# Kernel optimization log

Measured on AMD Instinct MI355X. Metric: run time of the kernel, lower is better.

The kernel has to match this reference:

```python
import jax, jax.numpy as jnp
import numpy as np

B, S, D, H = 2, 2048, 768, 12
DK = D // H


def setup_inputs() -> dict:
    key = jax.random.key(0)
    ks = jax.random.split(key, 10)
    sc = 0.02
    return {
        "k": jax.random.normal(ks[0], (B, S, D), jnp.float32),
        "q": jax.random.normal(ks[1], (B, S, D), jnp.float32),
        "v": jax.random.normal(ks[2], (B, S, D), jnp.float32),
        "mask": jnp.ones((B, 1, S, S), jnp.int32),
        "wq": jax.random.normal(ks[3], (D, D), jnp.float32) * sc,
        "bq": jnp.zeros((D,), jnp.float32),
        "wk": jax.random.normal(ks[4], (D, D), jnp.float32) * sc,
        "bk": jnp.zeros((D,), jnp.float32),
        "wv": jax.random.normal(ks[5], (D, D), jnp.float32) * sc,
        "bv": jnp.zeros((D,), jnp.float32),
        "wo": jax.random.normal(ks[6], (D, D), jnp.float32) * sc,
        "bo": jnp.zeros((D,), jnp.float32),
    }


def reference(k, q, v, mask, wq, bq, wk, bk, wv, bv, wo, bo):
    # Linear projections (torch Linear: x @ W^T + b)
    query = q @ wq.T + bq
    key_ = k @ wk.T + bk
    value = v @ wv.T + bv
    # [B,S,D] -> [B,H,S,DK]
    def split_heads(x):
        return x.reshape(B, S, H, DK).transpose(0, 2, 1, 3)
    Q, K, V = split_heads(query), split_heads(key_), split_heads(value)
    # NOTE: original masked_fill result is discarded -> mask is a no-op.
    scores = jnp.einsum("bhqd,bhkd->bhqk", Q, K) / jnp.sqrt(jnp.float32(DK))
    attn = jax.nn.softmax(scores, axis=-1)  # dropout p=0.0 -> identity
    out = jnp.einsum("bhqk,bhkd->bhqd", attn, V)
    out = out.transpose(0, 2, 1, 3).reshape(B, S, D)
    return out @ wo.T + bo
```

## Files before the change

kernel.cpp:

```cpp
#include <hip/hip_runtime.h>
#include <hip/hip_bf16.h>

#define B_  2
#define S_  2048
#define D_  768
#define H_  12
#define DK_ 64
#define NX_ (B_*S_*D_)
#define NW_ (D_*D_)
#define CSC 0.18033688011112042f

typedef __attribute__((ext_vector_type(8))) short  bf16x8;
typedef __attribute__((ext_vector_type(4))) float  f32x4;

__device__ __forceinline__ unsigned short f2bf(float f) {
    unsigned int u = __float_as_uint(f);
    u += 0x7fffu + ((u >> 16) & 1u);
    return (unsigned short)(u >> 16);
}

__device__ __forceinline__ unsigned cvtpk(float a, float b) {
    unsigned r;
    asm("v_cvt_pk_bf16_f32 %0, %1, %2" : "=v"(r) : "v"(a), "v"(b));
    return r;
}

__device__ __forceinline__ void async_cp16(const unsigned short* g,
                                           const unsigned short* lds_uniform_base) {
    __builtin_amdgcn_global_load_lds(
        (const __attribute__((address_space(1))) unsigned int*)(uintptr_t)g,
        (__attribute__((address_space(3))) unsigned int*)(unsigned int)(uintptr_t)lds_uniform_base,
        16, 0, 0);
}

struct CvtArgs { const float* s[7]; };

__global__ __launch_bounds__(256) void cvt_all(CvtArgs a,
                                               unsigned short* __restrict__ Xsw,
                                               unsigned short* __restrict__ Wsw) {
    const int bx = blockIdx.x;
    int y, inner;
    if (bx < 2304) { y = bx / 768;             inner = bx % 768; }
    else           { y = 3 + (bx - 2304) / 144; inner = (bx - 2304) % 144; }
    const int idx = inner * 256 + threadIdx.x;
    const int n  = idx / 48;
    const int g2 = idx % 48;
    const float* src = a.s[y] + (long)n * D_ + g2 * 16;
    const float zs = (y == 3) ? CSC : 1.0f;
    unsigned short o[16];
#pragma unroll
    for (int i = 0; i < 4; i++) {
        const float4 f = *(const float4*)(src + i * 4);
        o[i*4+0] = f2bf(f.x*zs); o[i*4+1] = f2bf(f.y*zs);
        o[i*4+2] = f2bf(f.z*zs); o[i*4+3] = f2bf(f.w*zs);
    }
    unsigned short* dst = (y >= 3) ? (Wsw + (long)(y - 3) * NW_ + (long)n * D_)
                                   : (Xsw + (long)y * NX_ + (long)n * D_);
    const int key = n & 7;
#pragma unroll
    for (int h = 0; h < 2; h++) {
        const int g8 = g2 * 2 + h;
        const int kdst = (g8 >> 3) * 64 + (((g8 & 7) ^ key) * 8);
        *(uint4*)(dst + kdst) = *(const uint4*)&o[h * 8];
    }
}

struct QkvArgs { const float* bias[3]; unsigned short* out[3]; };

__global__ __launch_bounds__(256, 3) void gemm_qkv(QkvArgs args,
                                                   const unsigned short* __restrict__ Xsw,
                                                   const unsigned short* __restrict__ Wsw) {
    __shared__ __align__(16) unsigned short smem[17408];
    unsigned short* As = smem;
    unsigned short* Bs = smem + 8192;

    const int t    = threadIdx.x;
    const int wave = t >> 6;
    const int lane = t & 63;
    const int l16  = lane & 15;
    const int quad = lane >> 4;
    const int wm   = wave >> 1, wn = wave & 1;
    const int m0   = blockIdx.x * 128;
    const int zz   = blockIdx.y / 6;
    const int nb   = blockIdx.y % 6;
    const int n0   = nb * 128;

    const unsigned short* Ap = Xsw + (long)zz * NX_;
    const unsigned short* Wp = Wsw + (long)zz * NW_;

    f32x4 acc[4][4];
#pragma unroll
    for (int s = 0; s < 4; s++)
#pragma unroll
        for (int j = 0; j < 4; j++) acc[s][j] = (f32x4){0.f, 0.f, 0.f, 0.f};

    const int lrow = lane >> 3;
    const int lcg  = lane & 7;

    for (int k0 = 0; k0 < D_; k0 += 64) {
        __syncthreads();
#pragma unroll
        for (int i = 0; i < 4; i++) {
            const int chunk = wave * 4 + i;
            async_cp16(Ap + (long)(m0 + chunk * 8 + lrow) * D_ + k0 + lcg * 8,
                       As + chunk * 512);
        }
#pragma unroll
        for (int i = 0; i < 4; i++) {
            const int chunk = wave * 4 + i;
            async_cp16(Wp + (long)(n0 + chunk * 8 + lrow) * D_ + k0 + lcg * 8,
                       Bs + chunk * 512);
        }
        __syncthreads();
#pragma unroll
        for (int ks = 0; ks < 2; ks++) {
            const int cg = ks * 4 + quad;
            bf16x8 af[4], bf[4];
#pragma unroll
            for (int s = 0; s < 4; s++) {
                const int r = wm * 64 + s * 16 + l16;
                af[s] = *(const bf16x8*)&As[r * 64 + ((cg ^ (r & 7)) * 8)];
            }
#pragma unroll
            for (int j = 0; j < 4; j++) {
                const int r = wn * 64 + j * 16 + l16;
                bf[j] = *(const bf16x8*)&Bs[r * 64 + ((cg ^ (r & 7)) * 8)];
            }
#pragma unroll
            for (int s = 0; s < 4; s++)
#pragma unroll
                for (int j = 0; j < 4; j++)
                    acc[s][j] = __builtin_amdgcn_mfma_f32_16x16x32_bf16(af[s], bf[j], acc[s][j], 0, 0, 0);
        }
    }
    __syncthreads();

    const int b     = m0 >> 11;
    const int sbase = m0 & (S_ - 1);
    const float zs  = (zz == 0) ? CSC : 1.0f;
    float bv[4];
#pragma unroll
    for (int j = 0; j < 4; j++) bv[j] = args.bias[zz][n0 + wn * 64 + j * 16 + l16] * zs;

    if (zz < 2) {
        unsigned short* Ls = smem;
#pragma unroll
        for (int s = 0; s < 4; s++)
#pragma unroll
            for (int j = 0; j < 4; j++)
#pragma unroll
                for (int r = 0; r < 4; r++)
                    Ls[(wm * 64 + s * 16 + quad * 4 + r) * 136 + wn * 64 + j * 16 + l16] =
                        f2bf(acc[s][j][r] + bv[j]);
        __syncthreads();
        const int row  = t >> 1;
        const int half = t & 1;
        unsigned short* Op = args.out[zz];
#pragma unroll
        for (int i = 0; i < 8; i++) {
            const int col  = half * 64 + i * 8;
            const int head = nb * 2 + half;
            const uint4 v = *(const uint4*)&Ls[row * 136 + col];
            *(uint4*)(Op + ((long)(b * H_ + head) * S_ + sbase + row) * DK_
                         + ((i ^ (row & 7)) * 8)) = v;
        }
    } else {
        unsigned short* Ls = smem;
#pragma unroll
        for (int s = 0; s < 4; s++)
#pragma unroll
            for (int j = 0; j < 4; j++)
#pragma unroll
                for (int r = 0; r < 4; r++) {
                    const int dk  = j * 16 + l16;
                    const int pos = wm * 64 + (s >> 1) * 32 + quad * 8 + (s & 1) * 4 + r;
                    Ls[wn * 8704 + dk * 136 + pos] = f2bf(acc[s][j][r] + bv[j]);
                }
        __syncthreads();
        const int rowIdx = t >> 1;
        const int hh = rowIdx >> 6, dk = rowIdx & 63;
        const int half = t & 1;
        unsigned short* Op = args.out[2];
#pragma unroll
        for (int i = 0; i < 8; i++) {
            const int col = half * 64 + i * 8;
            const uint4 v = *(const uint4*)&Ls[hh * 8704 + dk * 136 + col];
            const int head = nb * 2 + hh;
            *(uint4*)(Op + ((long)(b * H_ + head) * DK_ + dk) * S_
                         + sbase + half * 64 + ((i ^ (dk & 7)) * 8)) = v;
        }
    }
}

__global__ __launch_bounds__(256, 3) void attn_kernel(
    const unsigned short* __restrict__ Q, const unsigned short* __restrict__ K,
    const unsigned short* __restrict__ Vt, unsigned short* __restrict__ Ao)
{
    const int t    = threadIdx.x;
    const int wave = t >> 6;
    const int lane = t & 63;
    const int l16  = lane & 15;
    const int quad = lane >> 4;
    const int bid  = blockIdx.x;
    const int bh    = bid % 24;
    const int qtile = bid / 24;

    const unsigned short* Qp = Q  + (long)bh * S_ * DK_;
    const unsigned short* Kp = K  + (long)bh * S_ * DK_;
    const unsigned short* Vp = Vt + (long)bh * DK_ * S_;

    __shared__ __align__(16) unsigned short smem[16384];

    const int fkey = l16 & 7;
    const int fo0  = ((quad ^ fkey) * 8);
    const int fo1  = (((4 + quad) ^ fkey) * 8);

    bf16x8 qfrag[2];
    {
        const long qoff = (long)(qtile * 64 + wave * 16 + l16) * DK_;
        qfrag[0] = *(const bf16x8*)(Qp + qoff + fo0);
        qfrag[1] = *(const bf16x8*)(Qp + qoff + fo1);
    }

    const int ci0 = wave * 2;
    const int kd0 = ci0 * 512;
    const unsigned short* gk  = Kp + ci0 * 512 + lane * 8;
    const unsigned short* gv0 = Vp + (long)(ci0 * 8 + (lane >> 3)) * S_ + (lane & 7) * 8;
    const unsigned short* gv1 = gv0 + 8 * S_;

    async_cp16(gk,        smem + kd0);
    async_cp16(gk + 512,  smem + kd0 + 512);
    async_cp16(gv0,       smem + 8192 + kd0);
    async_cp16(gv1,       smem + 8192 + kd0 + 512);
    gk += 4096;  gv0 += 64;  gv1 += 64;

    f32x4 oacc[4];
#pragma unroll
    for (int j = 0; j < 4; j++) oacc[j] = (f32x4){0.f, 0.f, 0.f, 0.f};
    float lsum = 0.f;

    for (int it = 0; it < 32; ++it) {
        const int co = (it & 1) * 4096;
        const int no = 4096 - co;
        __syncthreads();
        const unsigned short* Ks = smem + co;
        const unsigned short* Vs = smem + 8192 + co;

        if (it < 31) {
            async_cp16(gk,        smem + no + kd0);
            async_cp16(gk + 512,  smem + no + kd0 + 512);
            async_cp16(gv0,       smem + 8192 + no + kd0);
            async_cp16(gv1,       smem + 8192 + no + kd0 + 512);
            gk += 4096;  gv0 += 64;  gv1 += 64;
        }

        f32x4 sacc[4];
#pragma unroll
        for (int j = 0; j < 4; j++) sacc[j] = (f32x4){0.f, 0.f, 0.f, 0.f};
#pragma unroll
        for (int ks = 0; ks < 2; ks++) {
            const int fo = ks ? fo1 : fo0;
            const bf16x8 qf = ks ? qfrag[1] : qfrag[0];
#pragma unroll
            for (int j = 0; j < 4; j++) {
                const bf16x8 bf = *(const bf16x8*)&Ks[(j * 16 + l16) * 64 + fo];
                sacc[j] = __builtin_amdgcn_mfma_f32_16x16x32_bf16(bf, qf, sacc[j], 0, 0, 0);
            }
        }

        float p[4][4];
#pragma unroll
        for (int j = 0; j < 4; j++)
#pragma unroll
            for (int r = 0; r < 4; r++)
                p[j][r] = exp2f(sacc[j][r]);
#pragma unroll
        for (int j = 0; j < 4; j++)
            lsum += (p[j][0] + p[j][1]) + (p[j][2] + p[j][3]);
        uint4 pw0, pw1;
        pw0.x = cvtpk(p[0][0], p[0][1]);  pw0.y = cvtpk(p[0][2], p[0][3]);
        pw0.z = cvtpk(p[1][0], p[1][1]);  pw0.w = cvtpk(p[1][2], p[1][3]);
        pw1.x = cvtpk(p[2][0], p[2][1]);  pw1.y = cvtpk(p[2][2], p[2][3]);
        pw1.z = cvtpk(p[3][0], p[3][1]);  pw1.w = cvtpk(p[3][2], p[3][3]);
        const bf16x8 pf0 = *(const bf16x8*)&pw0;
        const bf16x8 pf1 = *(const bf16x8*)&pw1;

#pragma unroll
        for (int ks = 0; ks < 2; ks++) {
            const int fo = ks ? fo1 : fo0;
            const bf16x8 pf = ks ? pf1 : pf0;
#pragma unroll
            for (int j = 0; j < 4; j++) {
                const bf16x8 vf = *(const bf16x8*)&Vs[(j * 16 + l16) * 64 + fo];
                oacc[j] = __builtin_amdgcn_mfma_f32_16x16x32_bf16(pf, vf, oacc[j], 0, 0, 0);
            }
        }
    }

    lsum += __shfl_xor(lsum, 16, 64);
    lsum += __shfl_xor(lsum, 32, 64);
    const float inv = 1.f / lsum;
    float scl[4];
#pragma unroll
    for (int r = 0; r < 4; r++) scl[r] = __shfl(inv, quad * 4 + r, 64);

    __syncthreads();
    unsigned short* Sc = smem;
#pragma unroll
    for (int j = 0; j < 4; j++)
#pragma unroll
        for (int r = 0; r < 4; r++) {
            const int row = wave * 16 + quad * 4 + r;
            const int c   = j * 2 + (l16 >> 3);
            Sc[row * 64 + ((c ^ (row & 7)) * 8) + (l16 & 7)] =
                f2bf(oacc[j][r] * scl[r]);
        }

    const int b = bh / H_, h = bh % H_;
    const int row = t >> 2;
    const int p0  = (t & 3) * 2;
    const int qrow = qtile * 64 + row;
    unsigned short* dst = Ao + (long)(b * S_ + qrow) * D_ + h * DK_;
    *(uint4*)(dst + p0 * 8)       = *(const uint4*)&Sc[row * 64 + p0 * 8];
    *(uint4*)(dst + (p0 + 1) * 8) = *(const uint4*)&Sc[row * 64 + (p0 + 1) * 8];
}

__global__ __launch_bounds__(256, 4) void gemm_out(
    const unsigned short* __restrict__ A, const unsigned short* __restrict__ Wsw,
    const float* __restrict__ bias, float* __restrict__ Out)
{
    __shared__ __align__(16) unsigned short smem[8704];
    unsigned short* As = smem;
    unsigned short* Bs = smem + 4096;

    const int t    = threadIdx.x;
    const int wave = t >> 6;
    const int lane = t & 63;
    const int l16  = lane & 15;
    const int quad = lane >> 4;
    const int wm   = wave >> 1, wn = wave & 1;
    const int m0   = blockIdx.x * 64;
    const int n0   = blockIdx.y * 64;

    f32x4 acc[2][2];
#pragma unroll
    for (int s = 0; s < 2; s++)
#pragma unroll
        for (int j = 0; j < 2; j++) acc[s][j] = (f32x4){0.f, 0.f, 0.f, 0.f};

    const int lrow = lane >> 3;
    const int lcg  = lane & 7;

    for (int k0 = 0; k0 < D_; k0 += 64) {
        __syncthreads();
#pragma unroll
        for (int i = 0; i < 2; i++) {
            const int chunk = wave * 2 + i;
            async_cp16(A + (long)(m0 + chunk * 8 + lrow) * D_ + k0 + lcg * 8,
                       As + chunk * 512);
        }
#pragma unroll
        for (int i = 0; i < 2; i++) {
            const int chunk = wave * 2 + i;
            async_cp16(Wsw + (long)(n0 + chunk * 8 + lrow) * D_ + k0 + lcg * 8,
                       Bs + chunk * 512);
        }
        __syncthreads();
#pragma unroll
        for (int ks = 0; ks < 2; ks++) {
            const int cg = ks * 4 + quad;
            bf16x8 af[2], bf[2];
#pragma unroll
            for (int s = 0; s < 2; s++) {
                const int r = wm * 32 + s * 16 + l16;
                af[s] = *(const bf16x8*)&As[r * 64 + ((cg ^ (r & 7)) * 8)];
            }
#pragma unroll
            for (int j = 0; j < 2; j++) {
                const int r = wn * 32 + j * 16 + l16;
                bf[j] = *(const bf16x8*)&Bs[r * 64 + ((cg ^ (r & 7)) * 8)];
            }
#pragma unroll
            for (int s = 0; s < 2; s++)
#pragma unroll
                for (int j = 0; j < 2; j++)
                    acc[s][j] = __builtin_amdgcn_mfma_f32_16x16x32_bf16(af[s], bf[j], acc[s][j], 0, 0, 0);
        }
    }

    float bv[2];
#pragma unroll
    for (int j = 0; j < 2; j++) bv[j] = bias[n0 + wn * 32 + j * 16 + l16];

    __syncthreads();
    float* fl = (float*)smem;
#pragma unroll
    for (int s = 0; s < 2; s++)
#pragma unroll
        for (int j = 0; j < 2; j++)
#pragma unroll
            for (int r = 0; r < 4; r++)
                fl[(wm * 32 + s * 16 + quad * 4 + r) * 67 + wn * 32 + j * 16 + l16] =
                    acc[s][j][r] + bv[j];
    __syncthreads();
    const int row = t >> 2, c0 = (t & 3) * 16;
#pragma unroll
    for (int i = 0; i < 4; i++) {
        const float4 v = *(const float4*)&fl[row * 67 + c0 + i * 4];
        *(float4*)(Out + (long)(m0 + row) * D_ + n0 + c0 + i * 4) = v;
    }
}

extern "C" void kernel_launch(void* const* d_in, const int* in_sizes, int n_in,
                              void* d_out, int out_size, void* d_ws, size_t ws_size,
                              hipStream_t stream) {
    const float* k_in = (const float*)d_in[0];
    const float* q_in = (const float*)d_in[1];
    const float* v_in = (const float*)d_in[2];
    const float* wq = (const float*)d_in[4];
    const float* bq = (const float*)d_in[5];
    const float* wk = (const float*)d_in[6];
    const float* bk = (const float*)d_in[7];
    const float* wv = (const float*)d_in[8];
    const float* bv = (const float*)d_in[9];
    const float* wo = (const float*)d_in[10];
    const float* bo = (const float*)d_in[11];

    unsigned short* ws = (unsigned short*)d_ws;
    unsigned short* Wsw = ws;
    unsigned short* Qb  = Wsw + 4ll * NW_;
    unsigned short* Kb  = Qb + (long)NX_;
    unsigned short* Vt  = Kb + (long)NX_;
    unsigned short* Xsw = Vt + (long)NX_;
    unsigned short* Ao  = Xsw;

    CvtArgs ca;
    ca.s[0] = q_in; ca.s[1] = k_in; ca.s[2] = v_in;
    ca.s[3] = wq;   ca.s[4] = wk;   ca.s[5] = wv;  ca.s[6] = wo;
    cvt_all<<<dim3(2880), 256, 0, stream>>>(ca, Xsw, Wsw);

    QkvArgs qa;
    qa.bias[0] = bq; qa.bias[1] = bk; qa.bias[2] = bv;
    qa.out[0] = Qb;  qa.out[1] = Kb;  qa.out[2] = Vt;
    gemm_qkv<<<dim3(32, 18), 256, 0, stream>>>(qa, Xsw, Wsw);

    attn_kernel<<<dim3(768), 256, 0, stream>>>(Qb, Kb, Vt, Ao);

    gemm_out<<<dim3(64, 12), 256, 0, stream>>>(Ao, Wsw + 3ll * NW_, bo, (float*)d_out);
}
```

Baseline: 205.5 us.

## Fuse activation fp32-to-bf16 conversion into QKV GEMM A-tile loads

The separate conversion kernel now only converts the four weight matrices. The QKV GEMM reads fp32 activations directly, packs them to bf16 in registers and writes them into swizzled LDS, replacing the async global-to-LDS copy of pre-converted activations. This removes a full write and re-read of the bf16 activation buffer. In exchange, each A tile is loaded synchronously through registers instead of asynchronously, every N-block re-reads fp32 data (twice the bytes), and rounding changes to a cheaper round-half-up pack.

```diff
diff --git a/kernel.cpp b/kernel.cpp
--- a/kernel.cpp
+++ b/kernel.cpp
@@ -19,6 +19,12 @@
     return (unsigned short)(u >> 16);
 }
 
+__device__ __forceinline__ unsigned pack_bf2(float a, float b) {
+    const unsigned ua = __float_as_uint(a) + 0x8000u;
+    const unsigned ub = __float_as_uint(b) + 0x8000u;
+    return __builtin_amdgcn_perm(ub, ua, 0x07060302u);
+}
+
 __device__ __forceinline__ unsigned cvtpk(float a, float b) {
     unsigned r;
     asm("v_cvt_pk_bf16_f32 %0, %1, %2" : "=v"(r) : "v"(a), "v"(b));
@@ -33,20 +39,17 @@
         16, 0, 0);
 }
 
-struct CvtArgs { const float* s[7]; };
-
-__global__ __launch_bounds__(256) void cvt_all(CvtArgs a,
-                                               unsigned short* __restrict__ Xsw,
-                                               unsigned short* __restrict__ Wsw) {
+struct CvtArgs { const float* s[4]; };
+
+__global__ __launch_bounds__(256) void cvt_w(CvtArgs a,
+                                             unsigned short* __restrict__ Wsw) {
     const int bx = blockIdx.x;
-    int y, inner;
-    if (bx < 2304) { y = bx / 768;             inner = bx % 768; }
-    else           { y = 3 + (bx - 2304) / 144; inner = (bx - 2304) % 144; }
+    const int y = bx / 144, inner = bx % 144;
     const int idx = inner * 256 + threadIdx.x;
     const int n  = idx / 48;
     const int g2 = idx % 48;
     const float* src = a.s[y] + (long)n * D_ + g2 * 16;
-    const float zs = (y == 3) ? CSC : 1.0f;
+    const float zs = (y == 0) ? CSC : 1.0f;
     unsigned short o[16];
 #pragma unroll
     for (int i = 0; i < 4; i++) {
@@ -54,8 +57,7 @@
         o[i*4+0] = f2bf(f.x*zs); o[i*4+1] = f2bf(f.y*zs);
         o[i*4+2] = f2bf(f.z*zs); o[i*4+3] = f2bf(f.w*zs);
     }
-    unsigned short* dst = (y >= 3) ? (Wsw + (long)(y - 3) * NW_ + (long)n * D_)
-                                   : (Xsw + (long)y * NX_ + (long)n * D_);
+    unsigned short* dst = Wsw + (long)y * NW_ + (long)n * D_;
     const int key = n & 7;
 #pragma unroll
     for (int h = 0; h < 2; h++) {
@@ -65,10 +67,9 @@
     }
 }
 
-struct QkvArgs { const float* bias[3]; unsigned short* out[3]; };
+struct QkvArgs { const float* a[3]; const float* bias[3]; unsigned short* out[3]; };
 
 __global__ __launch_bounds__(256, 3) void gemm_qkv(QkvArgs args,
-                                                   const unsigned short* __restrict__ Xsw,
                                                    const unsigned short* __restrict__ Wsw) {
     __shared__ __align__(16) unsigned short smem[17408];
     unsigned short* As = smem;
@@ -85,7 +86,7 @@
     const int nb   = blockIdx.y % 6;
     const int n0   = nb * 128;
 
-    const unsigned short* Ap = Xsw + (long)zz * NX_;
+    const float* Ap = args.a[zz];
     const unsigned short* Wp = Wsw + (long)zz * NW_;
 
     f32x4 acc[4][4];
@@ -97,19 +98,36 @@
     const int lrow = lane >> 3;
     const int lcg  = lane & 7;
 
+    const int arow = t >> 1;
+    const int ahalf = t & 1;
+    const float* asrc = Ap + (long)(m0 + arow) * D_ + ahalf * 32;
+    const int akey = arow & 7;
+    int aOff[4];
+#pragma unroll
+    for (int i = 0; i < 4; i++) {
+        const int c = ahalf * 4 + i;
+        aOff[i] = arow * 64 + ((c ^ akey) * 8);
+    }
+
     for (int k0 = 0; k0 < D_; k0 += 64) {
         __syncthreads();
-#pragma unroll
-        for (int i = 0; i < 4; i++) {
-            const int chunk = wave * 4 + i;
-            async_cp16(Ap + (long)(m0 + chunk * 8 + lrow) * D_ + k0 + lcg * 8,
-                       As + chunk * 512);
-        }
+        float4 av[8];
+#pragma unroll
+        for (int i = 0; i < 8; i++) av[i] = *(const float4*)(asrc + k0 + i * 4);
 #pragma unroll
         for (int i = 0; i < 4; i++) {
             const int chunk = wave * 4 + i;
             async_cp16(Wp + (long)(n0 + chunk * 8 + lrow) * D_ + k0 + lcg * 8,
                        Bs + chunk * 512);
+        }
+#pragma unroll
+        for (int i = 0; i < 4; i++) {
+            uint4 w;
+            w.x = pack_bf2(av[2*i].x,   av[2*i].y);
+            w.y = pack_bf2(av[2*i].z,   av[2*i].w);
+            w.z = pack_bf2(av[2*i+1].x, av[2*i+1].y);
+            w.w = pack_bf2(av[2*i+1].z, av[2*i+1].w);
+            *(uint4*)&As[aOff[i]] = w;
         }
         __syncthreads();
 #pragma unroll
@@ -431,18 +449,17 @@
     unsigned short* Qb  = Wsw + 4ll * NW_;
     unsigned short* Kb  = Qb + (long)NX_;
     unsigned short* Vt  = Kb + (long)NX_;
-    unsigned short* Xsw = Vt + (long)NX_;
-    unsigned short* Ao  = Xsw;
+    unsigned short* Ao  = Vt + (long)NX_;
 
     CvtArgs ca;
-    ca.s[0] = q_in; ca.s[1] = k_in; ca.s[2] = v_in;
-    ca.s[3] = wq;   ca.s[4] = wk;   ca.s[5] = wv;  ca.s[6] = wo;
-    cvt_all<<<dim3(2880), 256, 0, stream>>>(ca, Xsw, Wsw);
+    ca.s[0] = wq; ca.s[1] = wk; ca.s[2] = wv; ca.s[3] = wo;
+    cvt_w<<<dim3(576), 256, 0, stream>>>(ca, Wsw);
 
     QkvArgs qa;
+    qa.a[0] = q_in;  qa.a[1] = k_in;  qa.a[2] = v_in;
     qa.bias[0] = bq; qa.bias[1] = bk; qa.bias[2] = bv;
     qa.out[0] = Qb;  qa.out[1] = Kb;  qa.out[2] = Vt;
-    gemm_qkv<<<dim3(32, 18), 256, 0, stream>>>(qa, Xsw, Wsw);
+    gemm_qkv<<<dim3(32, 18), 256, 0, stream>>>(qa, Wsw);
 
     attn_kernel<<<dim3(768), 256, 0, stream>>>(Qb, Kb, Vt, Ao);
 
```

New measurement: 222.9 us. +8.5%, slower.
